# Kernel tuning notes

Hardware: AMD Instinct MI355X
Metric: run time of the kernel (lower is better)

The kernel has to match this reference:

```python
import jax, jax.numpy as jnp
import numpy as np

U_N = 100000
I_N = 50000
EMB_DIM = 64
L_N = 3          # number of propagation layers
NNZ = 4_800_000  # edges in the normalized bipartite graph (avg degree ~32)


def setup_inputs() -> dict:
    key = jax.random.key(0)
    k_u, k_i, k_r, k_c, k_v = jax.random.split(key, 5)
    N = U_N + I_N
    # Xavier-uniform-ish embedding init
    lim = float(np.sqrt(6.0 / (U_N + EMB_DIM)))
    user_emb = jax.random.uniform(k_u, (U_N, EMB_DIM), jnp.float32, -lim, lim)
    lim_i = float(np.sqrt(6.0 / (I_N + EMB_DIM)))
    item_emb = jax.random.uniform(k_i, (I_N, EMB_DIM), jnp.float32, -lim_i, lim_i)
    # COO sparse graph over all N = u_n + i_n nodes
    row = jax.random.randint(k_r, (NNZ,), 0, N, jnp.int32)
    col = jax.random.randint(k_c, (NNZ,), 0, N, jnp.int32)
    # emulate symmetric-normalized adjacency values ~ 1/deg so propagation stays bounded
    vals = jax.random.uniform(k_v, (NNZ,), jnp.float32) * (1.0 / 32.0)
    return {"user_emb": user_emb, "item_emb": item_emb, "row": row, "col": col, "vals": vals}


def reference(user_emb, item_emb, row, col, vals):
    N = user_emb.shape[0] + item_emb.shape[0]
    all_emb = jnp.concatenate([user_emb, item_emb], axis=0)  # [N, D]
    emb0 = all_emb
    acc = all_emb  # running sum over layer embeddings (layer 0 included)
    x = all_emb
    for _ in range(L_N):
        # SpMM: out[r] += vals[e] * x[col[e]] for each edge e with row[e] == r
        x = jax.ops.segment_sum(vals[:, None] * x[col], row, num_segments=N)
        acc = acc + x
    out = acc / (L_N + 1)  # mean over stacked layer embeddings
    return (emb0, out)
```

## Files before the change

kernel.cpp:

```cpp
#include <hip/hip_runtime.h>

#define U_N 100000
#define I_N 50000
#define N_NODES 150000
#define EMB_D 64
#define NNZ 4800000
#define ND (N_NODES * EMB_D)
#define ND4 (ND / 4)
#define UD4 (U_N * EMB_D / 4)

#define RPB 1024
#define NB ((N_NODES + RPB - 1) / RPB)
#define TILE 4096
#define NTILE ((NNZ + TILE - 1) / TILE)
#define HTILE 4096
#define NHT ((NNZ + HTILE - 1) / HTILE)

__device__ __forceinline__ unsigned short f2bf(float f) {
    unsigned int u = __float_as_uint(f);
    unsigned int r = (u + 0x7FFFu + ((u >> 16) & 1u)) >> 16;
    return (unsigned short)r;
}
__device__ __forceinline__ float bf2f(unsigned short h) {
    return __uint_as_float((unsigned int)h << 16);
}

__global__ void k_init(const float4* __restrict__ u, const float4* __restrict__ it,
                       float4* __restrict__ emb0, ushort4* __restrict__ hb0) {
    int i = blockIdx.x * blockDim.x + threadIdx.x;
    if (i >= ND4) return;
    float4 v = (i < UD4) ? u[i] : it[i - UD4];
    emb0[i] = v;
    ushort4 h;
    h.x = f2bf(v.x); h.y = f2bf(v.y); h.z = f2bf(v.z); h.w = f2bf(v.w);
    hb0[i] = h;
}

__global__ void k_bucket_hist(const int4* __restrict__ row4, int* __restrict__ bhist) {
    __shared__ int lh[4][NB];
    int t = threadIdx.x, wv = t >> 6;
    for (int i = t; i < 4 * NB; i += 256) ((int*)lh)[i] = 0;
    __syncthreads();
    int base = blockIdx.x * (HTILE / 4);
    int cnt = min(HTILE / 4, NNZ / 4 - base);
    for (int i = t; i < cnt; i += 256) {
        int4 r = row4[base + i];
        atomicAdd(&lh[wv][r.x >> 10], 1);
        atomicAdd(&lh[wv][r.y >> 10], 1);
        atomicAdd(&lh[wv][r.z >> 10], 1);
        atomicAdd(&lh[wv][r.w >> 10], 1);
    }
    __syncthreads();
    for (int i = t; i < NB; i += 256) {
        int s = lh[0][i] + lh[1][i] + lh[2][i] + lh[3][i];
        if (s) atomicAdd(&bhist[i], s);
    }
}

__global__ void k_bucket_scan(const int* __restrict__ bhist, int* __restrict__ bbase,
                              int* __restrict__ bcur) {
    __shared__ int wsum[4];
    int t = threadIdx.x, lane = t & 63, wv = t >> 6;
    int v = (t < NB) ? bhist[t] : 0;
    int iv = v;
    for (int off = 1; off < 64; off <<= 1) {
        int u = __shfl_up(iv, off);
        if (lane >= off) iv += u;
    }
    if (lane == 63) wsum[wv] = iv;
    __syncthreads();
    int woff = 0;
    for (int w = 0; w < wv; ++w) woff += wsum[w];
    int ex = woff + iv - v;
    if (t < NB) { bbase[t] = ex; bcur[t] = ex; }
    if (t == NB - 1) bbase[NB] = ex + v;
}

__global__ void k_partition(const int* __restrict__ row, const int* __restrict__ col,
                            const float* __restrict__ vals, int* __restrict__ bcur,
                            int2* __restrict__ tmp) {
    __shared__ int2 stage[TILE];
    __shared__ unsigned char stageB[TILE];
    __shared__ int whist[8][NB];
    __shared__ int cumw[8][NB];
    __shared__ int scn[NB];
    __shared__ int gbase[NB];
    __shared__ int wsum[8];
    int t = threadIdx.x;
    int lane = t & 63, wv = t >> 6;
    for (int i = t; i < 8 * NB; i += 512) ((int*)whist)[i] = 0;
    __syncthreads();
    int base = blockIdx.x * TILE;
    int cnt = min(TILE, NNZ - base);

    int  myb[8];
    int  myslot[8];
    int2 myp[8];
#pragma unroll
    for (int j = 0; j < 8; ++j) {
        int i = t + j * 512;
        myb[j] = -1;
        if (i < cnt) {
            int e = base + i;
            int r = row[e];
            int b = r >> 10;
            myb[j] = b;
            myp[j] = make_int2(((r & (RPB - 1)) << 18) | col[e], __float_as_int(vals[e]));
            myslot[j] = atomicAdd(&whist[wv][b], 1);
        }
    }
    __syncthreads();
    int v = 0;
    if (t < NB) {
        int run = 0;
#pragma unroll
        for (int w = 0; w < 8; ++w) {
            cumw[w][t] = run;
            run += whist[w][t];
        }
        v = run;
    }
    int iv = v;
    for (int off = 1; off < 64; off <<= 1) {
        int u = __shfl_up(iv, off);
        if (lane >= off) iv += u;
    }
    if (lane == 63) wsum[wv] = iv;
    __syncthreads();
    int woff = 0;
    for (int w = 0; w < wv; ++w) woff += wsum[w];
    if (t < NB) scn[t] = woff + iv - v;
    if (t < NB && v > 0) gbase[t] = atomicAdd(&bcur[t], v);
    __syncthreads();
#pragma unroll
    for (int j = 0; j < 8; ++j) {
        if (myb[j] >= 0) {
            int b = myb[j];
            int pos = scn[b] + cumw[wv][b] + myslot[j];
            stage[pos] = myp[j];
            stageB[pos] = (unsigned char)b;
        }
    }
    __syncthreads();
    for (int i = t; i < cnt; i += 512) {
        int b = stageB[i];
        tmp[gbase[b] + (i - scn[b])] = stage[i];
    }
}

__global__ void k_bucket_csr(const int* __restrict__ bbase, const int2* __restrict__ tmp,
                             int2* __restrict__ edges, int* __restrict__ rp) {
    __shared__ int ph[4][RPB];
    __shared__ int lex[RPB];
    __shared__ int wsum[16];
    int b = blockIdx.x, t = threadIdx.x;
    int lane = t & 63, wv = t >> 6;
    int s0 = bbase[b], s1 = bbase[b + 1];
    int n = s1 - s0;
    for (int i = t; i < 4 * RPB; i += 1024) ((int*)ph)[i] = 0;
    __syncthreads();
    int cp = wv >> 2;
    for (int i = t; i < n; i += 1024)
        atomicAdd(&ph[cp][(unsigned)tmp[s0 + i].x >> 18], 1);
    __syncthreads();
    int v = ph[0][t] + ph[1][t] + ph[2][t] + ph[3][t];
    int iv = v;
    for (int off = 1; off < 64; off <<= 1) {
        int u = __shfl_up(iv, off);
        if (lane >= off) iv += u;
    }
    if (lane == 63) wsum[wv] = iv;
    __syncthreads();
    int woff = 0;
    for (int w = 0; w < wv; ++w) woff += wsum[w];
    int excl = woff + iv - v;
    int r = b * RPB + t;
    if (r < N_NODES) rp[r] = s0 + excl;
    if (b == NB - 1 && t == 0) rp[N_NODES] = NNZ;
    lex[t] = s0 + excl;
    __syncthreads();
    for (int i = t; i < n; i += 1024) {
        int2 p = tmp[s0 + i];
        int rl = (unsigned)p.x >> 18;
        int pos = atomicAdd(&lex[rl], 1);
        edges[pos] = make_int2(p.x & 0x3FFFF, p.y);
    }
}

__device__ __forceinline__ float row_dot(const int* __restrict__ rp,
                                         const int2* __restrict__ edges,
                                         const unsigned short* __restrict__ x,
                                         int wid, int lane) {
    int start = __builtin_amdgcn_readfirstlane(rp[wid]);
    int end   = __builtin_amdgcn_readfirstlane(rp[wid + 1]);
    float s0 = 0.f, s1 = 0.f, s2 = 0.f, s3 = 0.f;
    int e = start;
    for (; e + 16 <= end; e += 16) {
        int2 E[16];
#pragma unroll
        for (int j = 0; j < 16; ++j) E[j] = edges[e + j];
        float g[16];
#pragma unroll
        for (int j = 0; j < 16; ++j) g[j] = bf2f(x[(size_t)E[j].x * EMB_D + lane]);
#pragma unroll
        for (int j = 0; j < 16; ++j) {
            float p = __int_as_float(E[j].y) * g[j];
            if ((j & 3) == 0) s0 += p;
            else if ((j & 3) == 1) s1 += p;
            else if ((j & 3) == 2) s2 += p;
            else s3 += p;
        }
    }
    int rem = end - e;
    if (rem > 0) {
        int2 E[16];
#pragma unroll
        for (int j = 0; j < 16; ++j) E[j] = edges[e + j];
#pragma unroll
        for (int j = 0; j < 16; ++j)
            if (j >= rem) { E[j].x = 0; E[j].y = 0; }
        float g[16];
#pragma unroll
        for (int j = 0; j < 16; ++j) g[j] = bf2f(x[(size_t)E[j].x * EMB_D + lane]);
#pragma unroll
        for (int j = 0; j < 16; ++j) {
            float p = __int_as_float(E[j].y) * g[j];
            if ((j & 3) == 0) s0 += p;
            else if ((j & 3) == 1) s1 += p;
            else if ((j & 3) == 2) s2 += p;
            else s3 += p;
        }
    }
    return (s0 + s1) + (s2 + s3);
}

__global__ void k_spmm_mid(const int* __restrict__ rp, const int2* __restrict__ edges,
                           const unsigned short* __restrict__ x,
                           unsigned short* __restrict__ y) {
    int wid = blockIdx.x * (blockDim.x >> 6) + (threadIdx.x >> 6);
    if (wid >= N_NODES) return;
    int lane = threadIdx.x & 63;
    float s = row_dot(rp, edges, x, wid, lane);
    y[(size_t)wid * EMB_D + lane] = f2bf(s);
}

__global__ void k_spmm_fin(const int* __restrict__ rp, const int2* __restrict__ edges,
                           const unsigned short* __restrict__ x,
                           const float* __restrict__ emb0,
                           const unsigned short* __restrict__ y1,
                           const unsigned short* __restrict__ y2,
                           float* __restrict__ acc) {
    int wid = blockIdx.x * (blockDim.x >> 6) + (threadIdx.x >> 6);
    if (wid >= N_NODES) return;
    int lane = threadIdx.x & 63;
    float s = row_dot(rp, edges, x, wid, lane);
    size_t o = (size_t)wid * EMB_D + lane;
    acc[o] = (emb0[o] + bf2f(y1[o]) + bf2f(y2[o]) + s) * 0.25f;
}

extern "C" void kernel_launch(void* const* d_in, const int* in_sizes, int n_in,
                              void* d_out, int out_size, void* d_ws, size_t ws_size,
                              hipStream_t stream) {
    const float* user_emb = (const float*)d_in[0];
    const float* item_emb = (const float*)d_in[1];
    const int*   row      = (const int*)d_in[2];
    const int*   col      = (const int*)d_in[3];
    const float* vals     = (const float*)d_in[4];

    float* emb0 = (float*)d_out;
    float* acc  = (float*)d_out + ND;

    int2* tmp   = (int2*)d_ws;
    int2* edges = tmp + NNZ;
    unsigned short* hb2 = (unsigned short*)(edges + NNZ);
    int*  ibase = (int*)(hb2 + ND);
    int*  rp    = ibase;
    int*  bhist = ibase + N_NODES + 1;
    int*  bbase = bhist + NB;
    int*  bcur  = bbase + NB + 1;
    unsigned short* hb0 = (unsigned short*)d_ws;
    unsigned short* hb1 = hb0 + ND;

    const int BLK = 256;
    const int grid_nd = (ND4 + BLK - 1) / BLK;
    const int grid_spmm = (N_NODES * 64 + BLK - 1) / BLK;

    hipMemsetAsync(bhist, 0, NB * sizeof(int), stream);
    k_bucket_hist<<<NHT, BLK, 0, stream>>>((const int4*)row, bhist);
    k_bucket_scan<<<1, BLK, 0, stream>>>(bhist, bbase, bcur);
    k_partition<<<NTILE, 512, 0, stream>>>(row, col, vals, bcur, tmp);
    k_bucket_csr<<<NB, 1024, 0, stream>>>(bbase, tmp, edges, rp);

    k_init<<<grid_nd, BLK, 0, stream>>>((const float4*)user_emb,
                                        (const float4*)item_emb,
                                        (float4*)emb0, (ushort4*)hb0);

    k_spmm_mid<<<grid_spmm, BLK, 0, stream>>>(rp, edges, hb0, hb1);
    k_spmm_mid<<<grid_spmm, BLK, 0, stream>>>(rp, edges, hb1, hb2);
    k_spmm_fin<<<grid_spmm, BLK, 0, stream>>>(rp, edges, hb2, emb0, hb1, hb2, acc);
}
```

Baseline: 570.7 us.

## Fuse init into histogram launch and split bucket CSR scatter across two blocks

Merges the embedding init/bf16 conversion kernel with the bucket histogram kernel into a single launch with a block-index split, which removes one launch and lets the two memory-bound jobs overlap. hb0 moves to a workspace region that does not alias tmp, so init can run before partition writes tmp. The CSR build kernel now launches two blocks per bucket. Both blocks count the whole bucket, and each scatters half of the edges, the second offset by counts from the first half. This doubles parallelism for the 147-block CSR stage but makes each block read the bucket's edges twice and adds an extra shared histogram.

After: 574.7 us. Within noise of the previous version (+0.7%).

```diff
diff --git a/kernel.cpp b/kernel.cpp
--- a/kernel.cpp
+++ b/kernel.cpp
@@ -15,6 +15,7 @@
 #define NTILE ((NNZ + TILE - 1) / TILE)
 #define HTILE 4096
 #define NHT ((NNZ + HTILE - 1) / HTILE)
+#define GRID_INIT ((ND4 + 255) / 256)
 
 __device__ __forceinline__ unsigned short f2bf(float f) {
     unsigned int u = __float_as_uint(f);
@@ -25,35 +26,37 @@
     return __uint_as_float((unsigned int)h << 16);
 }
 
-__global__ void k_init(const float4* __restrict__ u, const float4* __restrict__ it,
-                       float4* __restrict__ emb0, ushort4* __restrict__ hb0) {
-    int i = blockIdx.x * blockDim.x + threadIdx.x;
-    if (i >= ND4) return;
-    float4 v = (i < UD4) ? u[i] : it[i - UD4];
-    emb0[i] = v;
-    ushort4 h;
-    h.x = f2bf(v.x); h.y = f2bf(v.y); h.z = f2bf(v.z); h.w = f2bf(v.w);
-    hb0[i] = h;
-}
-
-__global__ void k_bucket_hist(const int4* __restrict__ row4, int* __restrict__ bhist) {
-    __shared__ int lh[4][NB];
-    int t = threadIdx.x, wv = t >> 6;
-    for (int i = t; i < 4 * NB; i += 256) ((int*)lh)[i] = 0;
-    __syncthreads();
-    int base = blockIdx.x * (HTILE / 4);
-    int cnt = min(HTILE / 4, NNZ / 4 - base);
-    for (int i = t; i < cnt; i += 256) {
-        int4 r = row4[base + i];
-        atomicAdd(&lh[wv][r.x >> 10], 1);
-        atomicAdd(&lh[wv][r.y >> 10], 1);
-        atomicAdd(&lh[wv][r.z >> 10], 1);
-        atomicAdd(&lh[wv][r.w >> 10], 1);
-    }
-    __syncthreads();
-    for (int i = t; i < NB; i += 256) {
-        int s = lh[0][i] + lh[1][i] + lh[2][i] + lh[3][i];
-        if (s) atomicAdd(&bhist[i], s);
+__global__ void k_init_hist(const float4* __restrict__ u, const float4* __restrict__ it,
+                            float4* __restrict__ emb0, ushort4* __restrict__ hb0,
+                            const int4* __restrict__ row4, int* __restrict__ bhist) {
+    int blk = blockIdx.x;
+    if (blk < GRID_INIT) {
+        int i = blk * 256 + threadIdx.x;
+        if (i >= ND4) return;
+        float4 v = (i < UD4) ? u[i] : it[i - UD4];
+        emb0[i] = v;
+        ushort4 h;
+        h.x = f2bf(v.x); h.y = f2bf(v.y); h.z = f2bf(v.z); h.w = f2bf(v.w);
+        hb0[i] = h;
+    } else {
+        __shared__ int lh[4][NB];
+        int t = threadIdx.x, wv = t >> 6;
+        for (int i = t; i < 4 * NB; i += 256) ((int*)lh)[i] = 0;
+        __syncthreads();
+        int base = (blk - GRID_INIT) * (HTILE / 4);
+        int cnt = min(HTILE / 4, NNZ / 4 - base);
+        for (int i = t; i < cnt; i += 256) {
+            int4 r = row4[base + i];
+            atomicAdd(&lh[wv][r.x >> 10], 1);
+            atomicAdd(&lh[wv][r.y >> 10], 1);
+            atomicAdd(&lh[wv][r.z >> 10], 1);
+            atomicAdd(&lh[wv][r.w >> 10], 1);
+        }
+        __syncthreads();
+        for (int i = t; i < NB; i += 256) {
+            int s = lh[0][i] + lh[1][i] + lh[2][i] + lh[3][i];
+            if (s) atomicAdd(&bhist[i], s);
+        }
     }
 }
 
@@ -151,17 +154,29 @@
 __global__ void k_bucket_csr(const int* __restrict__ bbase, const int2* __restrict__ tmp,
                              int2* __restrict__ edges, int* __restrict__ rp) {
     __shared__ int ph[4][RPB];
+    __shared__ int ha[2][RPB];
     __shared__ int lex[RPB];
     __shared__ int wsum[16];
-    int b = blockIdx.x, t = threadIdx.x;
-    int lane = t & 63, wv = t >> 6;
+    int bid = blockIdx.x;
+    int b = bid >> 1, s = bid & 1;
+    int t = threadIdx.x, lane = t & 63, wv = t >> 6;
     int s0 = bbase[b], s1 = bbase[b + 1];
     int n = s1 - s0;
+    int half = (n + 1) >> 1;
     for (int i = t; i < 4 * RPB; i += 1024) ((int*)ph)[i] = 0;
+    for (int i = t; i < 2 * RPB; i += 1024) ((int*)ha)[i] = 0;
     __syncthreads();
     int cp = wv >> 2;
-    for (int i = t; i < n; i += 1024)
-        atomicAdd(&ph[cp][(unsigned)tmp[s0 + i].x >> 18], 1);
+    if (s == 0) {
+        for (int i = t; i < n; i += 1024)
+            atomicAdd(&ph[cp][(unsigned)tmp[s0 + i].x >> 18], 1);
+    } else {
+        for (int i = t; i < n; i += 1024) {
+            int rl = (unsigned)tmp[s0 + i].x >> 18;
+            atomicAdd(&ph[cp][rl], 1);
+            if (i < half) atomicAdd(&ha[wv & 1][rl], 1);
+        }
+    }
     __syncthreads();
     int v = ph[0][t] + ph[1][t] + ph[2][t] + ph[3][t];
     int iv = v;
@@ -175,12 +190,16 @@
     for (int w = 0; w < wv; ++w) woff += wsum[w];
     int excl = woff + iv - v;
     int r = b * RPB + t;
-    if (r < N_NODES) rp[r] = s0 + excl;
-    if (b == NB - 1 && t == 0) rp[N_NODES] = NNZ;
-    lex[t] = s0 + excl;
-    __syncthreads();
-    for (int i = t; i < n; i += 1024) {
-        int2 p = tmp[s0 + i];
+    if (s == 0) {
+        if (r < N_NODES) rp[r] = s0 + excl;
+        if (b == NB - 1 && t == 0) rp[N_NODES] = NNZ;
+    }
+    lex[t] = s0 + excl + (s ? (ha[0][t] + ha[1][t]) : 0);
+    __syncthreads();
+    int e0 = s ? (s0 + half) : s0;
+    int e1 = s ? s1 : (s0 + half);
+    for (int i = e0 + t; i < e1; i += 1024) {
+        int2 p = tmp[i];
         int rl = (unsigned)p.x >> 18;
         int pos = atomicAdd(&lex[rl], 1);
         edges[pos] = make_int2(p.x & 0x3FFFF, p.y);
@@ -272,28 +291,25 @@
 
     int2* tmp   = (int2*)d_ws;
     int2* edges = tmp + NNZ;
-    unsigned short* hb2 = (unsigned short*)(edges + NNZ);
-    int*  ibase = (int*)(hb2 + ND);
+    unsigned short* hb0 = (unsigned short*)(edges + NNZ);
+    int*  ibase = (int*)(hb0 + ND);
     int*  rp    = ibase;
     int*  bhist = ibase + N_NODES + 1;
     int*  bbase = bhist + NB;
     int*  bcur  = bbase + NB + 1;
-    unsigned short* hb0 = (unsigned short*)d_ws;
-    unsigned short* hb1 = hb0 + ND;
+    unsigned short* hb1 = (unsigned short*)d_ws;
+    unsigned short* hb2 = hb1 + ND;
 
     const int BLK = 256;
-    const int grid_nd = (ND4 + BLK - 1) / BLK;
     const int grid_spmm = (N_NODES * 64 + BLK - 1) / BLK;
 
     hipMemsetAsync(bhist, 0, NB * sizeof(int), stream);
-    k_bucket_hist<<<NHT, BLK, 0, stream>>>((const int4*)row, bhist);
+    k_init_hist<<<GRID_INIT + NHT, BLK, 0, stream>>>(
+        (const float4*)user_emb, (const float4*)item_emb,
+        (float4*)emb0, (ushort4*)hb0, (const int4*)row, bhist);
     k_bucket_scan<<<1, BLK, 0, stream>>>(bhist, bbase, bcur);
     k_partition<<<NTILE, 512, 0, stream>>>(row, col, vals, bcur, tmp);
-    k_bucket_csr<<<NB, 1024, 0, stream>>>(bbase, tmp, edges, rp);
-
-    k_init<<<grid_nd, BLK, 0, stream>>>((const float4*)user_emb,
-                                        (const float4*)item_emb,
-                                        (float4*)emb0, (ushort4*)hb0);
+    k_bucket_csr<<<2 * NB, 1024, 0, stream>>>(bbase, tmp, edges, rp);
 
     k_spmm_mid<<<grid_spmm, BLK, 0, stream>>>(rp, edges, hb0, hb1);
     k_spmm_mid<<<grid_spmm, BLK, 0, stream>>>(rp, edges, hb1, hb2);
```
